# Optimization experiments

Hardware: AMD Instinct MI355X
Metric: run time of the kernel (lower is better)

The kernel has to match this reference:

```python
import jax, jax.numpy as jnp
import numpy as np
from jax import lax

B, C, D, H, W = 4, 256, 32, 32, 32
LATENT = 512


def setup_inputs() -> dict:
    key = jax.random.key(0)
    k = jax.random.split(key, 6)
    x = jax.random.normal(k[0], (B, C, D, H, W), dtype=jnp.float32)
    prev_rgb = jax.random.normal(k[1], (B, 1, D, H, W), dtype=jnp.float32)
    istyle = jax.random.normal(k[2], (B, LATENT), dtype=jnp.float32)
    # nn.Linear(latent_dim, input_channel): weight [C, LATENT], bias [C]
    lim = 1.0 / np.sqrt(LATENT)
    W_style = jax.random.uniform(k[3], (C, LATENT), minval=-lim, maxval=lim, dtype=jnp.float32)
    b_style = jax.random.uniform(k[4], (C,), minval=-lim, maxval=lim, dtype=jnp.float32)
    # Conv3DMod weight [out=1, C, 1,1,1], kaiming_normal fan_in, leaky_relu(a=0) gain=sqrt(2)
    conv_weight = jax.random.normal(k[5], (1, C, 1, 1, 1), dtype=jnp.float32) * np.float32(np.sqrt(2.0 / C))
    return {"x": x, "prev_rgb": prev_rgb, "istyle": istyle,
            "W_style": W_style, "b_style": b_style, "conv_weight": conv_weight}


def _blur3d(x):
    # kornia filter3d with normalized 3x3x3 [1,2,1] outer-product kernel, replicate padding
    f = jnp.array([1.0, 2.0, 1.0], dtype=x.dtype)
    ker = f[:, None, None] * f[None, :, None] * f[None, None, :]
    ker = (ker / ker.sum())[None, None]  # [1,1,3,3,3] (single channel)
    xp = jnp.pad(x, ((0, 0), (0, 0), (1, 1), (1, 1), (1, 1)), mode='edge')
    return lax.conv_general_dilated(
        xp, ker, window_strides=(1, 1, 1), padding='VALID',
        dimension_numbers=('NCDHW', 'OIDHW', 'NCDHW'))


def reference(x, prev_rgb, istyle, W_style, b_style, conv_weight):
    b, c, d, h, w = x.shape
    # to_style linear
    style = istyle @ W_style.T + b_style                    # [b, c]
    # Conv3DMod, kernel=1, demod=False: per-sample modulated weights reduce to a
    # per-(sample, channel) coefficient; conv is a channel-weighted sum.
    wk = conv_weight[0, :, 0, 0, 0]                         # [c]
    coef = wk[None, :] * (style + 1.0)                      # [b, c]
    out = jnp.einsum('bcdhw,bc->bdhw', x, coef)[:, None]    # [b,1,d,h,w]
    out = out + prev_rgb
    # Upsample scale=2, trilinear, align_corners=False (half-pixel centers)
    out = jax.image.resize(out, (b, 1, 2 * d, 2 * h, 2 * w), method='trilinear')
    out = _blur3d(out)
    return out
```

## Files before the change

### kernel.cpp

```cpp
#include <hip/hip_runtime.h>

#define BATCH 4
#define CH    256
#define SVOL  32768
#define SV4   8192
#define TILE  32
#define NCH   8
#define CCH   32

typedef float floatx4 __attribute__((ext_vector_type(4)));


__global__ void __launch_bounds__(256)
coef_kernel(const float* __restrict__ istyle,
            const float* __restrict__ W_style,
            const float* __restrict__ b_style,
            const float* __restrict__ wk,
            float* __restrict__ coef) {
    int tid  = threadIdx.x;
    int wave = blockIdx.x * 4 + (tid >> 6);
    int lane = tid & 63;
    int b = wave >> 8;
    int c = wave & 255;
    const float* is = istyle + b * 512;
    const float* wr = W_style + c * 512;
    float acc = 0.f;
    #pragma unroll
    for (int j = 0; j < 8; ++j) {
        int k = lane + j * 64;
        acc += is[k] * wr[k];
    }
    #pragma unroll
    for (int off = 32; off >= 1; off >>= 1)
        acc += __shfl_down(acc, off, 64);
    if (lane == 0)
        coef[b * 256 + c] = wk[c] * (acc + b_style[c] + 1.0f);
}

__global__ void __launch_bounds__(256)
reduce_c_kernel(const floatx4* __restrict__ x4,
                const float* __restrict__ coef,
                const floatx4* __restrict__ prev4,
                floatx4* __restrict__ small4) {
    __shared__ float   cf[CH];
    __shared__ floatx4 red[NCH][TILE];

    int t     = threadIdx.x;
    int pos   = t & (TILE - 1);
    int chunk = t >> 5;
    int gpos  = blockIdx.x * TILE + pos;
    int b     = gpos >> 13;
    int s4    = gpos & (SV4 - 1);

    cf[t] = coef[b * CH + t];
    __syncthreads();

    const floatx4* xp = x4 + (size_t)(b * CH + chunk * CCH) * SV4 + s4;
    floatx4 acc = {0.f, 0.f, 0.f, 0.f};
    #pragma unroll 16
    for (int cc = 0; cc < CCH; ++cc) {
        floatx4 v = __builtin_nontemporal_load(&xp[(size_t)cc * SV4]);
        float   w = cf[chunk * CCH + cc];
        acc += v * w;
    }
    red[chunk][pos] = acc;
    __syncthreads();

    if (t < TILE) {
        floatx4 r = prev4[gpos];
        #pragma unroll
        for (int k = 0; k < NCH; ++k)
            r += red[k][t];
        small4[gpos] = r;
    }
}

__global__ void __launch_bounds__(256)
upblur_kernel(const float* __restrict__ small,
              float* __restrict__ out) {
    int g  = blockIdx.x * 256 + threadIdx.x;
    int xo = g & 63;
    int yo = (g >> 6) & 63;
    int zo = (g >> 12) & 63;
    int b  = g >> 18;

    int jx = xo >> 1, jy = yo >> 1, jz = zo >> 1;
    int px = xo & 1,  py = yo & 1,  pz = zo & 1;

    int xi[3] = { jx > 0 ? jx - 1 : 0, jx, jx < 31 ? jx + 1 : 31 };
    int yi[3] = { jy > 0 ? jy - 1 : 0, jy, jy < 31 ? jy + 1 : 31 };
    int zi[3] = { jz > 0 ? jz - 1 : 0, jz, jz < 31 ? jz + 1 : 31 };

    float wx[3] = { px ? 1.f : 5.f, 10.f, px ? 5.f : 1.f };
    float wy[3] = { py ? 1.f : 5.f, 10.f, py ? 5.f : 1.f };
    float wz[3] = { pz ? 1.f : 5.f, 10.f, pz ? 5.f : 1.f };

    const float* base = small + (size_t)b * SVOL;
    float acc = 0.f;
    #pragma unroll
    for (int a = 0; a < 3; ++a) {
        const float* pzrow = base + zi[a] * 1024;
        float accy = 0.f;
        #pragma unroll
        for (int c = 0; c < 3; ++c) {
            const float* pyrow = pzrow + yi[c] * 32;
            float row = wx[0] * pyrow[xi[0]] + wx[1] * pyrow[xi[1]] + wx[2] * pyrow[xi[2]];
            accy += wy[c] * row;
        }
        acc += wz[a] * accy;
    }
    out[g] = acc * (1.0f / 4096.0f);
}

extern "C" void kernel_launch(void* const* d_in, const int* in_sizes, int n_in,
                              void* d_out, int out_size, void* d_ws, size_t ws_size,
                              hipStream_t stream) {
    const float* x       = (const float*)d_in[0];
    const float* prev    = (const float*)d_in[1];
    const float* istyle  = (const float*)d_in[2];
    const float* W_style = (const float*)d_in[3];
    const float* b_style = (const float*)d_in[4];
    const float* wk      = (const float*)d_in[5];
    float* ws    = (float*)d_ws;
    float* coef  = ws;
    float* small = ws + 1024;

    coef_kernel<<<256, 256, 0, stream>>>(istyle, W_style, b_style, wk, coef);

    reduce_c_kernel<<<BATCH * SV4 / TILE, 256, 0, stream>>>(
        (const floatx4*)x, coef, (const floatx4*)prev, (floatx4*)small);

    upblur_kernel<<<BATCH * 64 * 64 * 64 / 256, 256, 0, stream>>>(small, (float*)d_out);
}
```

Before: 195.9 us.

## Compute 2x2x2 output block per thread in upblur and widen reduce tile

The upsample+blur kernel now has each thread handle one coarse voxel and emit all eight fine outputs. It loads the 27-point neighbourhood once and shares separable partial sums across the eight parity combinations, written as floatx2 stores. This removes redundant gathers and per-output index math. The channel-reduction kernel is also retuned to 64 positions per block with 4 channel chunks of 64, halving block count and the LDS reduction width.

Result: no change. 196.3 us (+0.2%).

```diff
diff --git a/kernel.cpp b/kernel.cpp
--- a/kernel.cpp
+++ b/kernel.cpp
@@ -4,11 +4,12 @@
 #define CH    256
 #define SVOL  32768
 #define SV4   8192
-#define TILE  32
-#define NCH   8
-#define CCH   32
+#define TILE  64
+#define NCH   4
+#define CCH   64
 
 typedef float floatx4 __attribute__((ext_vector_type(4)));
+typedef float floatx2 __attribute__((ext_vector_type(2)));
 
 
 __global__ void __launch_bounds__(256)
@@ -47,7 +48,7 @@
 
     int t     = threadIdx.x;
     int pos   = t & (TILE - 1);
-    int chunk = t >> 5;
+    int chunk = t >> 6;
     int gpos  = blockIdx.x * TILE + pos;
     int b     = gpos >> 13;
     int s4    = gpos & (SV4 - 1);
@@ -78,38 +79,62 @@
 __global__ void __launch_bounds__(256)
 upblur_kernel(const float* __restrict__ small,
               float* __restrict__ out) {
-    int g  = blockIdx.x * 256 + threadIdx.x;
-    int xo = g & 63;
-    int yo = (g >> 6) & 63;
-    int zo = (g >> 12) & 63;
-    int b  = g >> 18;
+    int u  = blockIdx.x * 256 + threadIdx.x;
+    int jx = u & 31;
+    int jy = (u >> 5) & 31;
+    int jz = (u >> 10) & 31;
+    int b  = u >> 15;
 
-    int jx = xo >> 1, jy = yo >> 1, jz = zo >> 1;
-    int px = xo & 1,  py = yo & 1,  pz = zo & 1;
-
-    int xi[3] = { jx > 0 ? jx - 1 : 0, jx, jx < 31 ? jx + 1 : 31 };
-    int yi[3] = { jy > 0 ? jy - 1 : 0, jy, jy < 31 ? jy + 1 : 31 };
-    int zi[3] = { jz > 0 ? jz - 1 : 0, jz, jz < 31 ? jz + 1 : 31 };
-
-    float wx[3] = { px ? 1.f : 5.f, 10.f, px ? 5.f : 1.f };
-    float wy[3] = { py ? 1.f : 5.f, 10.f, py ? 5.f : 1.f };
-    float wz[3] = { pz ? 1.f : 5.f, 10.f, pz ? 5.f : 1.f };
+    int xm = jx > 0 ? jx - 1 : 0, xp_ = jx < 31 ? jx + 1 : 31;
+    int ym = jy > 0 ? jy - 1 : 0, yp_ = jy < 31 ? jy + 1 : 31;
+    int zm = jz > 0 ? jz - 1 : 0, zp_ = jz < 31 ? jz + 1 : 31;
+    int zi[3] = { zm, jz, zp_ };
+    int yi[3] = { ym, jy, yp_ };
+    int xi[3] = { xm, jx, xp_ };
 
     const float* base = small + (size_t)b * SVOL;
-    float acc = 0.f;
+
+    float ex[3][3], ox[3][3];
     #pragma unroll
     for (int a = 0; a < 3; ++a) {
-        const float* pzrow = base + zi[a] * 1024;
-        float accy = 0.f;
+        const float* pz = base + zi[a] * 1024;
         #pragma unroll
         for (int c = 0; c < 3; ++c) {
-            const float* pyrow = pzrow + yi[c] * 32;
-            float row = wx[0] * pyrow[xi[0]] + wx[1] * pyrow[xi[1]] + wx[2] * pyrow[xi[2]];
-            accy += wy[c] * row;
+            const float* py = pz + yi[c] * 32;
+            float v0 = py[xi[0]], v1 = py[xi[1]], v2 = py[xi[2]];
+            float m = 10.f * v1;
+            ex[a][c] = 5.f * v0 + m + v2;
+            ox[a][c] = v0 + m + 5.f * v2;
         }
-        acc += wz[a] * accy;
     }
-    out[g] = acc * (1.0f / 4096.0f);
+    float eye[3], eyo[3], oye[3], oyo[3];
+    #pragma unroll
+    for (int a = 0; a < 3; ++a) {
+        float me = 10.f * ex[a][1], mo = 10.f * ox[a][1];
+        eye[a] = 5.f * ex[a][0] + me + ex[a][2];
+        eyo[a] = 5.f * ox[a][0] + mo + ox[a][2];
+        oye[a] = ex[a][0] + me + 5.f * ex[a][2];
+        oyo[a] = ox[a][0] + mo + 5.f * ox[a][2];
+    }
+    const float s = 1.0f / 4096.0f;
+    float z0ee = (5.f * eye[0] + 10.f * eye[1] + eye[2]) * s;
+    float z0eo = (5.f * eyo[0] + 10.f * eyo[1] + eyo[2]) * s;
+    float z0oe = (5.f * oye[0] + 10.f * oye[1] + oye[2]) * s;
+    float z0oo = (5.f * oyo[0] + 10.f * oyo[1] + oyo[2]) * s;
+    float z1ee = (eye[0] + 10.f * eye[1] + 5.f * eye[2]) * s;
+    float z1eo = (eyo[0] + 10.f * eyo[1] + 5.f * eyo[2]) * s;
+    float z1oe = (oye[0] + 10.f * oye[1] + 5.f * oye[2]) * s;
+    float z1oo = (oyo[0] + 10.f * oyo[1] + 5.f * oyo[2]) * s;
+
+    size_t obase = (size_t)b * 262144 + (size_t)(2 * jz) * 4096 + (size_t)(2 * jy) * 64 + 2 * jx;
+    floatx2* o0 = (floatx2*)(out + obase);
+    floatx2* o1 = (floatx2*)(out + obase + 64);
+    floatx2* o2 = (floatx2*)(out + obase + 4096);
+    floatx2* o3 = (floatx2*)(out + obase + 4160);
+    *o0 = (floatx2){z0ee, z0eo};
+    *o1 = (floatx2){z0oe, z0oo};
+    *o2 = (floatx2){z1ee, z1eo};
+    *o3 = (floatx2){z1oe, z1oo};
 }
 
 extern "C" void kernel_launch(void* const* d_in, const int* in_sizes, int n_in,
@@ -130,5 +155,5 @@
     reduce_c_kernel<<<BATCH * SV4 / TILE, 256, 0, stream>>>(
         (const floatx4*)x, coef, (const floatx4*)prev, (floatx4*)small);
 
-    upblur_kernel<<<BATCH * 64 * 64 * 64 / 256, 256, 0, stream>>>(small, (float*)d_out);
+    upblur_kernel<<<BATCH * 32768 / 256, 256, 0, stream>>>(small, (float*)d_out);
 }
```
